# Performance work log

Measured on AMD Instinct MI355X. Metric: run time of the kernel, lower is better.

## Reference

```python
import jax, jax.numpy as jnp
import numpy as np

D = 768       # input_dim / model width
H = 3072      # expert hidden width (init arg 'output_dim')
E = 8         # num_experts
K = 2         # top_k
NOISE_STD = 0.1
B, S = 2, 1024


def setup_inputs() -> dict:
    key = jax.random.key(0)
    ks = jax.random.split(key, 16)
    sd = lambda fan_in: 1.0 / np.sqrt(fan_in)
    return {
        "x": jax.random.normal(ks[0], (B, S, D), dtype=jnp.float32),
        "noise": jax.random.normal(ks[1], (B, S, E), dtype=jnp.float32),
        # router
        "Wr": jax.random.normal(ks[2], (D, E), dtype=jnp.float32) * sd(D),
        "br": jnp.zeros((E,), dtype=jnp.float32),
        # stacked expert FFNs: d -> h -> d
        "W1": jax.random.normal(ks[3], (E, D, H), dtype=jnp.float32) * sd(D),
        "b1": jnp.zeros((E, H), dtype=jnp.float32),
        "W2": jax.random.normal(ks[4], (E, H, D), dtype=jnp.float32) * sd(H),
        "b2": jnp.zeros((E, D), dtype=jnp.float32),
        # shared expert
        "Ws1": jax.random.normal(ks[5], (D, H), dtype=jnp.float32) * sd(D),
        "bs1": jnp.zeros((H,), dtype=jnp.float32),
        "Ws2": jax.random.normal(ks[6], (H, D), dtype=jnp.float32) * sd(H),
        "bs2": jnp.zeros((D,), dtype=jnp.float32),
        # mixing scalars (alpha trainable, beta frozen in torch)
        "alpha": jnp.float32(0.3),
        "beta": jnp.float32(0.7),
    }


def reference(x, noise, Wr, br, W1, b1, W2, b2, Ws1, bs1, Ws2, bs2, alpha, beta):
    b, s, d = x.shape
    xt = x.reshape(-1, d)                       # [T, D]
    nt = noise.reshape(-1, E)                   # [T, E]
    T = xt.shape[0]

    # router: noisy logits -> top-k -> softmax over selected experts only
    logits = xt @ Wr + br + NOISE_STD * nt      # [T, E]
    top_vals, top_idx = jax.lax.top_k(logits, K)  # [T, K]
    top_w = jax.nn.softmax(top_vals, axis=-1)     # softmax over -inf-masked logits == softmax over top-k
    gates = jnp.zeros((T, E), dtype=x.dtype).at[jnp.arange(T)[:, None], top_idx].set(top_w)  # [T, E], 0 elsewhere

    # experts (dense over E; non-selected contributions are zeroed by gates)
    h = jax.nn.leaky_relu(jnp.einsum('td,edh->teh', xt, W1) + b1, negative_slope=0.01)  # [T, E, H]
    y = jnp.einsum('teh,ehd->ted', h, W2) + b2                                          # [T, E, D]
    moe_out = jnp.einsum('ted,te->td', y, gates)                                        # [T, D]

    # shared expert
    sh = jax.nn.leaky_relu(xt @ Ws1 + bs1, negative_slope=0.01)
    shared_out = sh @ Ws2 + bs2                                                         # [T, D]

    w = jax.nn.softmax(jnp.stack([alpha, beta]))
    out = shared_out * w[0] + moe_out * w[1]
    return out.reshape(b, s, d)
```

## Files before the change

kernel.cpp:

```cpp
#include <hip/hip_runtime.h>
#include <hip/hip_bf16.h>
#include <cstdio>
#include <cstdint>

#define TNUM 2048
#define DDIM 768
#define HDIM 3072
#define ENUM 8

typedef __attribute__((ext_vector_type(8))) __bf16 bf16x8;
typedef __attribute__((ext_vector_type(4))) float f32x4;
typedef __attribute__((ext_vector_type(8))) unsigned short ushort8_t;

__device__ __forceinline__ unsigned short f2bf(float f) {
    __bf16 h = (__bf16)f;
    unsigned short u;
    __builtin_memcpy(&u, &h, 2);
    return u;
}

__device__ __forceinline__ void async_cp16(const unsigned short* g, unsigned short* l) {
    __builtin_amdgcn_global_load_lds((const __attribute__((address_space(1))) void*)g,
                                     (__attribute__((address_space(3))) void*)l,
                                     16, 0, 0);
}

__global__ void cast_x_kernel(const float* __restrict__ x, unsigned short* __restrict__ xb) {
    int i = (blockIdx.x * 256 + threadIdx.x) * 8;
    float4 a = *(const float4*)(x + i);
    float4 b = *(const float4*)(x + i + 4);
    ushort4 lo = make_ushort4(f2bf(a.x), f2bf(a.y), f2bf(a.z), f2bf(a.w));
    ushort4 hi = make_ushort4(f2bf(b.x), f2bf(b.y), f2bf(b.z), f2bf(b.w));
    *(ushort4*)(xb + i) = lo;
    *(ushort4*)(xb + i + 4) = hi;
}

__global__ __launch_bounds__(256)
void transw_kernel(const float* __restrict__ W1, const float* __restrict__ W2,
                   const float* __restrict__ Ws1, const float* __restrict__ Ws2,
                   unsigned short* __restrict__ W1t, unsigned short* __restrict__ W2t,
                   unsigned short* __restrict__ Ws1t, unsigned short* __restrict__ Ws2t) {
    int z = blockIdx.z;
    const float* in; unsigned short* out; int R, C;
    if (z < 8)       { in = W1 + (size_t)z * DDIM * HDIM; out = W1t + (size_t)z * HDIM * DDIM; R = DDIM; C = HDIM; }
    else if (z < 16) { int e = z - 8; in = W2 + (size_t)e * HDIM * DDIM; out = W2t + (size_t)e * DDIM * HDIM; R = HDIM; C = DDIM; }
    else if (z == 16){ in = Ws1; out = Ws1t; R = DDIM; C = HDIM; }
    else             { in = Ws2; out = Ws2t; R = HDIM; C = DDIM; }
    int nx = C / 128;
    int c0 = (blockIdx.x % nx) * 128, r0 = (blockIdx.x / nx) * 128;
    __shared__ unsigned short tileT[128 * 136];
    int tid = threadIdx.x;
    int l15 = tid & 15;
    #pragma unroll
    for (int p = 0; p < 16; p++) {
        int unit = p * 16 + (tid >> 4);
        int r = unit >> 1, hf = unit & 1;
        int cb = hf * 64 + l15 * 4;
        float4 v = *(const float4*)(in + (size_t)(r0 + r) * C + c0 + cb);
        tileT[(cb + 0) * 136 + r] = f2bf(v.x);
        tileT[(cb + 1) * 136 + r] = f2bf(v.y);
        tileT[(cb + 2) * 136 + r] = f2bf(v.z);
        tileT[(cb + 3) * 136 + r] = f2bf(v.w);
    }
    __syncthreads();
    #pragma unroll
    for (int p = 0; p < 8; p++) {
        int cc = p * 16 + (tid >> 4);
        ushort8_t u = *(const ushort8_t*)&tileT[cc * 136 + l15 * 8];
        *(ushort8_t*)(out + (size_t)(c0 + cc) * R + r0 + l15 * 8) = u;
    }
}

__global__ void router_kernel(const float* __restrict__ x, const float* __restrict__ noise,
                              const float* __restrict__ Wr, const float* __restrict__ br,
                              int* __restrict__ counts, int* __restrict__ list,
                              int* __restrict__ inv, float* __restrict__ tokp) {
    int lane = threadIdx.x & 63;
    int t = blockIdx.x * 4 + (threadIdx.x >> 6);
    float acc[8];
    #pragma unroll
    for (int e = 0; e < 8; e++) acc[e] = 0.f;
    #pragma unroll
    for (int i = 0; i < 12; i++) {
        int d = i * 64 + lane;
        float xv = x[t * DDIM + d];
        float4 w0 = *(const float4*)(Wr + d * 8);
        float4 w1 = *(const float4*)(Wr + d * 8 + 4);
        acc[0] += xv * w0.x; acc[1] += xv * w0.y; acc[2] += xv * w0.z; acc[3] += xv * w0.w;
        acc[4] += xv * w1.x; acc[5] += xv * w1.y; acc[6] += xv * w1.z; acc[7] += xv * w1.w;
    }
    #pragma unroll
    for (int e = 0; e < 8; e++) {
        #pragma unroll
        for (int off2 = 32; off2 >= 1; off2 >>= 1)
            acc[e] += __shfl_xor(acc[e], off2, 64);
    }
    if (lane == 0) {
        float lg[8];
        #pragma unroll
        for (int e = 0; e < 8; e++) lg[e] = acc[e] + br[e] + 0.1f * noise[t * 8 + e];
        int e0 = 0;
        #pragma unroll
        for (int e = 1; e < 8; e++) if (lg[e] > lg[e0]) e0 = e;
        int e1 = -1;
        #pragma unroll
        for (int e = 0; e < 8; e++) if (e != e0 && (e1 < 0 || lg[e] > lg[e1])) e1 = e;
        float m = fmaxf(lg[e0], lg[e1]);
        float p0 = expf(lg[e0] - m), p1 = expf(lg[e1] - m);
        float inv_s = 1.f / (p0 + p1);
        int s0 = atomicAdd(&counts[e0], 1);
        list[e0 * TNUM + s0] = t;
        int s1 = atomicAdd(&counts[e1], 1);
        list[e1 * TNUM + s1] = t;
        inv[t * 2 + 0] = (e0 << 16) | s0;
        inv[t * 2 + 1] = (e1 << 16) | s1;
        tokp[t * 2 + 0] = p0 * inv_s;
        tokp[t * 2 + 1] = p1 * inv_s;
    }
}

__global__ void finalize_kernel(const int* __restrict__ counts, int* __restrict__ offs,
                                const float* __restrict__ alpha, const float* __restrict__ beta,
                                float* __restrict__ scal) {
    int s = 0;
    for (int e = 0; e < 8; e++) { offs[e] = s; s += counts[e]; }
    offs[8] = s;
    float a = alpha[0], b = beta[0];
    float m = fmaxf(a, b);
    float ea = expf(a - m), eb = expf(b - m);
    float inv = 1.f / (ea + eb);
    scal[0] = ea * inv;
    scal[1] = eb * inv;
}


__global__ __launch_bounds__(256, 4)
void ffn1_kernel(const unsigned short* __restrict__ xb,
                 const unsigned short* __restrict__ W1t,
                 const unsigned short* __restrict__ Ws1t,
                 const float* __restrict__ b1, const float* __restrict__ bs1,
                 const int* __restrict__ counts, const int* __restrict__ offs,
                 const int* __restrict__ list,
                 unsigned short* __restrict__ hbuf) {
    int j = blockIdx.z * 8 + blockIdx.x;
    if (j >= 20) return;
    int y = blockIdx.y;
    int mt = y / 12, ntl = y % 12;
    int cnt, hbase, n0, m0;
    const unsigned short* Bmat;
    const float* bias;
    const int* lst = nullptr;
    if (j < 16) {
        int e = j >> 1, nh = j & 1;
        cnt = counts[e];
        m0 = mt * 128;
        if (m0 >= cnt) return;
        hbase = offs[e];
        n0 = nh * 1536 + ntl * 128;
        Bmat = W1t + (size_t)e * HDIM * DDIM;
        bias = b1 + e * HDIM;
        lst = list + e * TNUM;
    } else {
        int q = j - 16;
        int mh = q >> 1, nh = q & 1;
        if (mt >= 8) return;
        m0 = mh * 1024 + mt * 128;
        cnt = 1 << 30;
        hbase = 2 * TNUM;
        n0 = nh * 1536 + ntl * 128;
        Bmat = Ws1t;
        bias = bs1;
    }

    __shared__ __align__(16) unsigned short As[2][512 * 8];
    __shared__ __align__(16) unsigned short Bs[2][512 * 8];

    int tid = threadIdx.x;
    int w = tid >> 6, lane = tid & 63;
    int l15 = lane & 15, quad = lane >> 4;
    int wm = (w & 1) * 64, wn = (w >> 1) * 64;

    const unsigned short* gA[2];
    const unsigned short* gB[2];
    int ldsoff[2];
    #pragma unroll
    for (int r = 0; r < 2; r++) {
        int rc = r * 4 + w;
        int rowl = rc * 16 + l15;
        int row;
        if (lst) row = lst[min(m0 + rowl, cnt - 1)];
        else     row = m0 + rowl;
        gA[r] = xb + (size_t)row * DDIM + quad * 8;
        gB[r] = Bmat + (size_t)(n0 + rowl) * DDIM + quad * 8;
        ldsoff[r] = rc * 512;
    }

    f32x4 zero = {0.f, 0.f, 0.f, 0.f};
    f32x4 acc[4][4];
    #pragma unroll
    for (int i = 0; i < 4; i++)
        #pragma unroll
        for (int jj = 0; jj < 4; jj++) acc[i][jj] = zero;

    int rcA = (w & 1) * 4;
    int rcB = (w >> 1) * 4;

    #pragma unroll
    for (int r = 0; r < 2; r++) {
        async_cp16(gA[r], &As[0][ldsoff[r]]);
        async_cp16(gB[r], &Bs[0][ldsoff[r]]);
    }

    #pragma unroll 1
    for (int kt = 0; kt < DDIM / 32; kt++) {
        __syncthreads();
        int cur = kt & 1;
        if (kt + 1 < DDIM / 32) {
            int ko = (kt + 1) * 32;
            #pragma unroll
            for (int r = 0; r < 2; r++) {
                async_cp16(gA[r] + ko, &As[cur ^ 1][ldsoff[r]]);
                async_cp16(gB[r] + ko, &Bs[cur ^ 1][ldsoff[r]]);
            }
        }
        bf16x8 af[4], bv[4];
        #pragma unroll
        for (int i = 0; i < 4; i++)
            af[i] = *(const bf16x8*)&As[cur][((rcA + i) * 64 + quad * 16 + l15) * 8];
        #pragma unroll
        for (int jj = 0; jj < 4; jj++)
            bv[jj] = *(const bf16x8*)&Bs[cur][((rcB + jj) * 64 + quad * 16 + l15) * 8];
        #pragma unroll
        for (int i = 0; i < 4; i++)
            #pragma unroll
            for (int jj = 0; jj < 4; jj++)
                acc[i][jj] = __builtin_amdgcn_mfma_f32_16x16x32_bf16(af[i], bv[jj], acc[i][jj], 0, 0, 0);
    }

    #pragma unroll
    for (int i = 0; i < 4; i++) {
        int rbase = m0 + wm + i * 16 + quad * 4;
        #pragma unroll
        for (int jj = 0; jj < 4; jj++) {
            int gc = n0 + wn + jj * 16 + l15;
            float bvl = bias[gc];
            #pragma unroll
            for (int r = 0; r < 4; r++) {
                int gr = rbase + r;
                if (gr < cnt) {
                    float v = acc[i][jj][r] + bvl;
                    v = v > 0.f ? v : 0.01f * v;
                    hbuf[(size_t)(hbase + gr) * HDIM + gc] = f2bf(v);
                }
            }
        }
    }
}

__global__ __launch_bounds__(256, 4)
void ffn2_kernel(const unsigned short* __restrict__ hbuf,
                 const unsigned short* __restrict__ W2t,
                 const unsigned short* __restrict__ Ws2t,
                 const int* __restrict__ counts, const int* __restrict__ offs,
                 float* __restrict__ ybuf) {
    int j = blockIdx.z * 8 + blockIdx.x;
    int y = blockIdx.y;
    int mt = y / 6, ntl = y % 6;
    int cnt, hbase, m0, kh;
    const unsigned short* Bmat;
    if (j < 16) {
        int e = j >> 1; kh = j & 1;
        cnt = counts[e];
        m0 = mt * 64;
        if (m0 >= cnt) return;
        hbase = offs[e];
        Bmat = W2t + (size_t)e * DDIM * HDIM;
    } else {
        int q = j - 16;
        int mh = q >> 1; kh = q & 1;
        if (mt >= 8) return;
        m0 = mh * 512 + mt * 64;
        cnt = 1 << 30;
        hbase = 2 * TNUM;
        Bmat = Ws2t;
    }
    int n0 = ntl * 128;
    int kbase = kh * (HDIM / 2);

    __shared__ __align__(16) unsigned short As[2][256 * 8];
    __shared__ __align__(16) unsigned short Bs[2][512 * 8];

    int tid = threadIdx.x;
    int w = tid >> 6, lane = tid & 63;
    int l15 = lane & 15, quad = lane >> 4;
    int wm = (w & 1) * 32, wn = (w >> 1) * 64;

    int rowl = w * 16 + l15;
    int ra = (j < 16) ? min(m0 + rowl, cnt - 1) : (m0 + rowl);
    const unsigned short* gA0 = hbuf + (size_t)(hbase + ra) * HDIM + kbase + quad * 8;
    unsigned short* lA0base0 = (unsigned short*)&As[0][w * 512];
    unsigned short* lA0base1 = (unsigned short*)&As[1][w * 512];

    const unsigned short* gB[2];
    int ldsoffB[2];
    #pragma unroll
    for (int r = 0; r < 2; r++) {
        int rc = r * 4 + w;
        gB[r] = Bmat + (size_t)(n0 + rc * 16 + l15) * HDIM + kbase + quad * 8;
        ldsoffB[r] = rc * 512;
    }

    f32x4 zero = {0.f, 0.f, 0.f, 0.f};
    f32x4 acc[2][4];
    #pragma unroll
    for (int i = 0; i < 2; i++)
        #pragma unroll
        for (int jj = 0; jj < 4; jj++) acc[i][jj] = zero;

    int rcA = (w & 1) * 2;
    int rcB = (w >> 1) * 4;

    async_cp16(gA0, lA0base0);
    #pragma unroll
    for (int r = 0; r < 2; r++) async_cp16(gB[r], &Bs[0][ldsoffB[r]]);

    const int KT = (HDIM / 2) / 32;
    #pragma unroll 1
    for (int kt = 0; kt < KT; kt++) {
        __syncthreads();
        int cur = kt & 1;
        if (kt + 1 < KT) {
            int ko = (kt + 1) * 32;
            async_cp16(gA0 + ko, cur ? lA0base0 : lA0base1);
            #pragma unroll
            for (int r = 0; r < 2; r++) async_cp16(gB[r] + ko, &Bs[cur ^ 1][ldsoffB[r]]);
        }
        bf16x8 af[2], bv[4];
        #pragma unroll
        for (int i = 0; i < 2; i++)
            af[i] = *(const bf16x8*)&As[cur][((rcA + i) * 64 + quad * 16 + l15) * 8];
        #pragma unroll
        for (int jj = 0; jj < 4; jj++)
            bv[jj] = *(const bf16x8*)&Bs[cur][((rcB + jj) * 64 + quad * 16 + l15) * 8];
        #pragma unroll
        for (int i = 0; i < 2; i++)
            #pragma unroll
            for (int jj = 0; jj < 4; jj++)
                acc[i][jj] = __builtin_amdgcn_mfma_f32_16x16x32_bf16(af[i], bv[jj], acc[i][jj], 0, 0, 0);
    }

    float* yb = ybuf + (size_t)kh * 6144 * DDIM;
    #pragma unroll
    for (int i = 0; i < 2; i++) {
        int rbase = m0 + wm + i * 16 + quad * 4;
        #pragma unroll
        for (int r = 0; r < 4; r++) {
            int gr = rbase + r;
            if (gr >= cnt) continue;
            float* orow = yb + (size_t)(hbase + gr) * DDIM + n0 + wn;
            #pragma unroll
            for (int jj = 0; jj < 4; jj++)
                orow[jj * 16 + l15] = acc[i][jj][r];
        }
    }
}

__global__ void mix_kernel(const float* __restrict__ ybuf, const int* __restrict__ inv,
                           const float* __restrict__ tokp, const int* __restrict__ offs,
                           const float* __restrict__ b2, const float* __restrict__ bs2,
                           const float* __restrict__ scal, float* __restrict__ out) {
    int t = blockIdx.x;
    int c = threadIdx.x * 4;
    int i0 = inv[t * 2 + 0], i1 = inv[t * 2 + 1];
    int e0 = i0 >> 16, sl0 = i0 & 0xFFFF;
    int e1 = i1 >> 16, sl1 = i1 & 0xFFFF;
    float p0 = tokp[t * 2 + 0], p1 = tokp[t * 2 + 1];
    float ws = scal[0], wmx = scal[1];
    size_t rA = (size_t)(offs[e0] + sl0) * DDIM + c;
    size_t rB = (size_t)(offs[e1] + sl1) * DDIM + c;
    size_t rS = (size_t)(2 * TNUM + t) * DDIM + c;
    const float* y0 = ybuf;
    const float* y1 = ybuf + (size_t)6144 * DDIM;
    float4 vA0 = *(const float4*)(y0 + rA);
    float4 vA1 = *(const float4*)(y1 + rA);
    float4 vB0 = *(const float4*)(y0 + rB);
    float4 vB1 = *(const float4*)(y1 + rB);
    float4 vS0 = *(const float4*)(y0 + rS);
    float4 vS1 = *(const float4*)(y1 + rS);
    float4 bA = *(const float4*)(b2 + e0 * DDIM + c);
    float4 bB = *(const float4*)(b2 + e1 * DDIM + c);
    float4 bS = *(const float4*)(bs2 + c);
    float4 o;
    o.x = ws * (vS0.x + vS1.x + bS.x) + wmx * (p0 * (vA0.x + vA1.x + bA.x) + p1 * (vB0.x + vB1.x + bB.x));
    o.y = ws * (vS0.y + vS1.y + bS.y) + wmx * (p0 * (vA0.y + vA1.y + bA.y) + p1 * (vB0.y + vB1.y + bB.y));
    o.z = ws * (vS0.z + vS1.z + bS.z) + wmx * (p0 * (vA0.z + vA1.z + bA.z) + p1 * (vB0.z + vB1.z + bB.z));
    o.w = ws * (vS0.w + vS1.w + bS.w) + wmx * (p0 * (vA0.w + vA1.w + bA.w) + p1 * (vB0.w + vB1.w + bB.w));
    *(float4*)(out + (size_t)t * DDIM + c) = o;
}

extern "C" void kernel_launch(void* const* d_in, const int* in_sizes, int n_in,
                              void* d_out, int out_size, void* d_ws, size_t ws_size,
                              hipStream_t stream) {
    const float* x     = (const float*)d_in[0];
    const float* noise = (const float*)d_in[1];
    const float* Wr    = (const float*)d_in[2];
    const float* br    = (const float*)d_in[3];
    const float* W1    = (const float*)d_in[4];
    const float* b1    = (const float*)d_in[5];
    const float* W2    = (const float*)d_in[6];
    const float* b2    = (const float*)d_in[7];
    const float* Ws1   = (const float*)d_in[8];
    const float* bs1   = (const float*)d_in[9];
    const float* Ws2   = (const float*)d_in[10];
    const float* bs2   = (const float*)d_in[11];
    const float* alpha = (const float*)d_in[12];
    const float* beta  = (const float*)d_in[13];

    char* ws = (char*)d_ws;
    size_t off = 0;
    auto alloc = [&](size_t bytes) -> char* {
        char* p = ws + off;
        off = (off + bytes + 255) & ~(size_t)255;
        return p;
    };
    int*   counts = (int*)  alloc(ENUM * 4);
    int*   offs   = (int*)  alloc(16 * 4);
    float* scal   = (float*)alloc(2 * 4);
    int*   list   = (int*)  alloc((size_t)ENUM * TNUM * 4);
    int*   inv    = (int*)  alloc((size_t)TNUM * 2 * 4);
    float* tokp   = (float*)alloc((size_t)TNUM * 2 * 4);
    unsigned short* xb   = (unsigned short*)alloc((size_t)TNUM * DDIM * 2);
    unsigned short* W1t  = (unsigned short*)alloc((size_t)ENUM * HDIM * DDIM * 2);
    unsigned short* Ws1t = (unsigned short*)alloc((size_t)HDIM * DDIM * 2);
    unsigned short* W2t  = (unsigned short*)alloc((size_t)ENUM * DDIM * HDIM * 2);
    unsigned short* Ws2t = (unsigned short*)alloc((size_t)DDIM * HDIM * 2);
    unsigned short* hbuf = (unsigned short*)alloc((size_t)(3 * TNUM) * HDIM * 2);
    float* ybuf = (float*)W1t;
    if (off > ws_size) {
        fprintf(stderr, "kernel_launch: workspace too small (need %zu, have %zu)\n", off, ws_size);
        return;
    }

    hipMemsetAsync(counts, 0, ENUM * 4, stream);

    cast_x_kernel<<<dim3((TNUM * DDIM / 8) / 256), dim3(256), 0, stream>>>(x, xb);
    transw_kernel<<<dim3(144, 1, 18), dim3(256), 0, stream>>>(W1, W2, Ws1, Ws2, W1t, W2t, Ws1t, Ws2t);
    router_kernel<<<dim3(TNUM / 4), dim3(256), 0, stream>>>(x, noise, Wr, br, counts, list, inv, tokp);
    finalize_kernel<<<dim3(1), dim3(1), 0, stream>>>(counts, offs, alpha, beta, scal);
    ffn1_kernel<<<dim3(8, 192, 3), dim3(256), 0, stream>>>(xb, W1t, Ws1t, b1, bs1, counts, offs, list, hbuf);
    ffn2_kernel<<<dim3(8, 192, 3), dim3(256), 0, stream>>>(hbuf, W2t, Ws2t, counts, offs, ybuf);
    mix_kernel<<<dim3(TNUM), dim3(192), 0, stream>>>(ybuf, inv, tokp, offs, b2, bs2, scal, (float*)d_out);
}
```

Before: 491.9 us.

## Triple-buffer FFN GEMM pipelines, persist M-tiles, and swizzle weight transpose LDS

Both expert GEMM kernels move from a double-buffered to a triple-buffered LDS pipeline with explicit vmcnt waits, so two K-slices are in flight at once. Grids shrink from 192 to 48 Y-blocks, and each block now loops over several M-tiles instead of launching one block per tile and exiting early on empty tiles. The weight transpose kernel packs bf16 pairs through lane shuffles and writes 32-bit words into a swizzled LDS tile to avoid bank conflicts. The costs are more LDS per block and lower occupancy (launch bounds drop from 4 to 3), plus less parallelism on experts that receive few tokens.

Result: faster. 462.3 us (-6.0%).

```diff
diff --git a/kernel.cpp b/kernel.cpp
--- a/kernel.cpp
+++ b/kernel.cpp
@@ -7,6 +7,9 @@
 #define DDIM 768
 #define HDIM 3072
 #define ENUM 8
+
+#define WAITVM(N) asm volatile("s_waitcnt vmcnt(" #N ")" ::: "memory")
+#define MEMFENCE() asm volatile("" ::: "memory")
 
 typedef __attribute__((ext_vector_type(8))) __bf16 bf16x8;
 typedef __attribute__((ext_vector_type(4))) float f32x4;
@@ -48,26 +51,45 @@
     else             { in = Ws2; out = Ws2t; R = HDIM; C = DDIM; }
     int nx = C / 128;
     int c0 = (blockIdx.x % nx) * 128, r0 = (blockIdx.x / nx) * 128;
-    __shared__ unsigned short tileT[128 * 136];
+    __shared__ __align__(16) unsigned int tileT32[128 * 68];
     int tid = threadIdx.x;
     int l15 = tid & 15;
+    int g = tid >> 4;
+    int par = (g >> 1) & 1;
+    int hf = g & 1;
+    int cb = hf * 64 + l15 * 4;
     #pragma unroll
     for (int p = 0; p < 16; p++) {
-        int unit = p * 16 + (tid >> 4);
-        int r = unit >> 1, hf = unit & 1;
-        int cb = hf * 64 + l15 * 4;
+        int unit = p * 16 + g;
+        int r = unit >> 1;
         float4 v = *(const float4*)(in + (size_t)(r0 + r) * C + c0 + cb);
-        tileT[(cb + 0) * 136 + r] = f2bf(v.x);
-        tileT[(cb + 1) * 136 + r] = f2bf(v.y);
-        tileT[(cb + 2) * 136 + r] = f2bf(v.z);
-        tileT[(cb + 3) * 136 + r] = f2bf(v.w);
+        unsigned int m01 = (unsigned int)f2bf(v.x) | ((unsigned int)f2bf(v.y) << 16);
+        unsigned int m23 = (unsigned int)f2bf(v.z) | ((unsigned int)f2bf(v.w) << 16);
+        unsigned int o01 = __shfl_xor(m01, 32);
+        unsigned int o23 = __shfl_xor(m23, 32);
+        unsigned int wA = par ? ((o23 & 0xffffu) | (m23 << 16))
+                              : ((m01 & 0xffffu) | (o01 << 16));
+        unsigned int wB = par ? ((o23 >> 16) | (m23 & 0xffff0000u))
+                              : ((m01 >> 16) | (o01 & 0xffff0000u));
+        int ca = cb + par * 2;
+        int rp = unit >> 2;
+        int cq = ca >> 2;
+        int woff = 4 * (((rp >> 2) + 3 * cq) & 15) + (((rp & 3) + cq) & 3);
+        tileT32[ca * 68 + woff] = wA;
+        tileT32[(ca + 1) * 68 + woff] = wB;
     }
     __syncthreads();
     #pragma unroll
     for (int p = 0; p < 8; p++) {
-        int cc = p * 16 + (tid >> 4);
-        ushort8_t u = *(const ushort8_t*)&tileT[cc * 136 + l15 * 8];
-        *(ushort8_t*)(out + (size_t)(c0 + cc) * R + r0 + l15 * 8) = u;
+        int cc = p * 16 + g;
+        int cqp = cc >> 2;
+        const uint4 W = *(const uint4*)&tileT32[cc * 68 + 4 * ((l15 + 3 * cqp) & 15)];
+        unsigned int a0 = W.x, a1 = W.y, a2 = W.z, a3 = W.w;
+        int rsel = cqp & 3;
+        if (rsel & 1) { unsigned int t = a0; a0 = a1; a1 = a2; a2 = a3; a3 = t; }
+        if (rsel & 2) { unsigned int t0 = a0, t1 = a1; a0 = a2; a1 = a3; a2 = t0; a3 = t1; }
+        uint4 ov; ov.x = a0; ov.y = a1; ov.z = a2; ov.w = a3;
+        *(uint4*)(out + (size_t)(c0 + cc) * R + r0 + l15 * 8) = ov;
     }
 }
 
@@ -134,7 +156,7 @@
 }
 
 
-__global__ __launch_bounds__(256, 4)
+__global__ __launch_bounds__(256, 3)
 void ffn1_kernel(const unsigned short* __restrict__ xb,
                  const unsigned short* __restrict__ W1t,
                  const unsigned short* __restrict__ Ws1t,
@@ -143,18 +165,17 @@
                  const int* __restrict__ list,
                  unsigned short* __restrict__ hbuf) {
     int j = blockIdx.z * 8 + blockIdx.x;
-    if (j >= 20) return;
     int y = blockIdx.y;
-    int mt = y / 12, ntl = y % 12;
-    int cnt, hbase, n0, m0;
+    int mt0 = y / 12, ntl = y % 12;
+    int cnt, hbase, n0, mbase, ntiles;
     const unsigned short* Bmat;
     const float* bias;
     const int* lst = nullptr;
     if (j < 16) {
         int e = j >> 1, nh = j & 1;
         cnt = counts[e];
-        m0 = mt * 128;
-        if (m0 >= cnt) return;
+        ntiles = (cnt + 127) >> 7;
+        mbase = 0;
         hbase = offs[e];
         n0 = nh * 1536 + ntl * 128;
         Bmat = W1t + (size_t)e * HDIM * DDIM;
@@ -162,95 +183,111 @@
         lst = list + e * TNUM;
     } else {
         int q = j - 16;
-        int mh = q >> 1, nh = q & 1;
-        if (mt >= 8) return;
-        m0 = mh * 1024 + mt * 128;
+        int ms = q >> 1, nh = q & 1;
+        mbase = ms * 512;
+        ntiles = 4;
         cnt = 1 << 30;
         hbase = 2 * TNUM;
         n0 = nh * 1536 + ntl * 128;
         Bmat = Ws1t;
         bias = bs1;
     }
-
-    __shared__ __align__(16) unsigned short As[2][512 * 8];
-    __shared__ __align__(16) unsigned short Bs[2][512 * 8];
+    if (mt0 >= ntiles) return;
+
+    __shared__ __align__(16) unsigned short As[3][512 * 8];
+    __shared__ __align__(16) unsigned short Bs[3][512 * 8];
 
     int tid = threadIdx.x;
     int w = tid >> 6, lane = tid & 63;
     int l15 = lane & 15, quad = lane >> 4;
     int wm = (w & 1) * 64, wn = (w >> 1) * 64;
 
-    const unsigned short* gA[2];
     const unsigned short* gB[2];
     int ldsoff[2];
+    int rowl[2];
     #pragma unroll
     for (int r = 0; r < 2; r++) {
         int rc = r * 4 + w;
-        int rowl = rc * 16 + l15;
-        int row;
-        if (lst) row = lst[min(m0 + rowl, cnt - 1)];
-        else     row = m0 + rowl;
-        gA[r] = xb + (size_t)row * DDIM + quad * 8;
-        gB[r] = Bmat + (size_t)(n0 + rowl) * DDIM + quad * 8;
+        rowl[r] = rc * 16 + l15;
+        gB[r] = Bmat + (size_t)(n0 + rowl[r]) * DDIM + quad * 8;
         ldsoff[r] = rc * 512;
     }
-
-    f32x4 zero = {0.f, 0.f, 0.f, 0.f};
-    f32x4 acc[4][4];
-    #pragma unroll
-    for (int i = 0; i < 4; i++)
-        #pragma unroll
-        for (int jj = 0; jj < 4; jj++) acc[i][jj] = zero;
-
     int rcA = (w & 1) * 4;
     int rcB = (w >> 1) * 4;
-
-    #pragma unroll
-    for (int r = 0; r < 2; r++) {
-        async_cp16(gA[r], &As[0][ldsoff[r]]);
-        async_cp16(gB[r], &Bs[0][ldsoff[r]]);
-    }
-
-    #pragma unroll 1
-    for (int kt = 0; kt < DDIM / 32; kt++) {
-        __syncthreads();
-        int cur = kt & 1;
-        if (kt + 1 < DDIM / 32) {
-            int ko = (kt + 1) * 32;
+    const int KT = DDIM / 32;
+
+    for (int mt = mt0; mt < ntiles; mt += 4) {
+        int m0 = mbase + mt * 128;
+        const unsigned short* gA[2];
+        #pragma unroll
+        for (int r = 0; r < 2; r++) {
+            int row;
+            if (lst) row = lst[min(m0 + rowl[r], cnt - 1)];
+            else     row = m0 + rowl[r];
+            gA[r] = xb + (size_t)row * DDIM + quad * 8;
+        }
+
+        f32x4 zero = {0.f, 0.f, 0.f, 0.f};
+        f32x4 acc[4][4];
+        #pragma unroll
+        for (int i = 0; i < 4; i++)
+            #pragma unroll
+            for (int jj = 0; jj < 4; jj++) acc[i][jj] = zero;
+
+        __builtin_amdgcn_s_barrier();
+        MEMFENCE();
+        #pragma unroll
+        for (int t = 0; t < 2; t++)
             #pragma unroll
             for (int r = 0; r < 2; r++) {
-                async_cp16(gA[r] + ko, &As[cur ^ 1][ldsoff[r]]);
-                async_cp16(gB[r] + ko, &Bs[cur ^ 1][ldsoff[r]]);
+                async_cp16(gA[r] + t * 32, &As[t][ldsoff[r]]);
+                async_cp16(gB[r] + t * 32, &Bs[t][ldsoff[r]]);
             }
-        }
-        bf16x8 af[4], bv[4];
-        #pragma unroll
-        for (int i = 0; i < 4; i++)
-            af[i] = *(const bf16x8*)&As[cur][((rcA + i) * 64 + quad * 16 + l15) * 8];
-        #pragma unroll
-        for (int jj = 0; jj < 4; jj++)
-            bv[jj] = *(const bf16x8*)&Bs[cur][((rcB + jj) * 64 + quad * 16 + l15) * 8];
-        #pragma unroll
-        for (int i = 0; i < 4; i++)
+
+        #pragma unroll 1
+        for (int kt = 0; kt < KT; kt++) {
+            if (kt == KT - 1) { WAITVM(0); } else { WAITVM(4); }
+            __builtin_amdgcn_s_barrier();
+            MEMFENCE();
+            int cur = kt % 3;
+            if (kt + 2 < KT) {
+                int nb = (kt + 2) % 3;
+                int ko = (kt + 2) * 32;
+                #pragma unroll
+                for (int r = 0; r < 2; r++) {
+                    async_cp16(gA[r] + ko, &As[nb][ldsoff[r]]);
+                    async_cp16(gB[r] + ko, &Bs[nb][ldsoff[r]]);
+                }
+            }
+            bf16x8 af[4], bv[4];
+            #pragma unroll
+            for (int i = 0; i < 4; i++)
+                af[i] = *(const bf16x8*)&As[cur][((rcA + i) * 64 + quad * 16 + l15) * 8];
             #pragma unroll
             for (int jj = 0; jj < 4; jj++)
-                acc[i][jj] = __builtin_amdgcn_mfma_f32_16x16x32_bf16(af[i], bv[jj], acc[i][jj], 0, 0, 0);
-    }
-
-    #pragma unroll
-    for (int i = 0; i < 4; i++) {
-        int rbase = m0 + wm + i * 16 + quad * 4;
-        #pragma unroll
-        for (int jj = 0; jj < 4; jj++) {
-            int gc = n0 + wn + jj * 16 + l15;
-            float bvl = bias[gc];
-            #pragma unroll
-            for (int r = 0; r < 4; r++) {
-                int gr = rbase + r;
-                if (gr < cnt) {
-                    float v = acc[i][jj][r] + bvl;
-                    v = v > 0.f ? v : 0.01f * v;
-                    hbuf[(size_t)(hbase + gr) * HDIM + gc] = f2bf(v);
+                bv[jj] = *(const bf16x8*)&Bs[cur][((rcB + jj) * 64 + quad * 16 + l15) * 8];
+            #pragma unroll
+            for (int i = 0; i < 4; i++)
+                #pragma unroll
+                for (int jj = 0; jj < 4; jj++)
+                    acc[i][jj] = __builtin_amdgcn_mfma_f32_16x16x32_bf16(af[i], bv[jj], acc[i][jj], 0, 0, 0);
+        }
+
+        #pragma unroll
+        for (int i = 0; i < 4; i++) {
+            int rbase = m0 + wm + i * 16 + quad * 4;
+            #pragma unroll
+            for (int jj = 0; jj < 4; jj++) {
+                int gc = n0 + wn + jj * 16 + l15;
+                float bvl = bias[gc];
+                #pragma unroll
+                for (int r = 0; r < 4; r++) {
+                    int gr = rbase + r;
+                    if (gr < cnt) {
+                        float v = acc[i][jj][r] + bvl;
+                        v = v > 0.f ? v : 0.01f * v;
+                        hbuf[(size_t)(hbase + gr) * HDIM + gc] = f2bf(v);
+                    }
                 }
             }
         }
@@ -265,42 +302,37 @@
                  float* __restrict__ ybuf) {
     int j = blockIdx.z * 8 + blockIdx.x;
     int y = blockIdx.y;
-    int mt = y / 6, ntl = y % 6;
-    int cnt, hbase, m0, kh;
+    int mt0 = y / 6, ntl = y % 6;
+    int cnt, hbase, mbase, kh, ntiles;
     const unsigned short* Bmat;
     if (j < 16) {
         int e = j >> 1; kh = j & 1;
         cnt = counts[e];
-        m0 = mt * 64;
-        if (m0 >= cnt) return;
+        ntiles = (cnt + 63) >> 6;
+        mbase = 0;
         hbase = offs[e];
         Bmat = W2t + (size_t)e * DDIM * HDIM;
     } else {
         int q = j - 16;
         int mh = q >> 1; kh = q & 1;
-        if (mt >= 8) return;
-        m0 = mh * 512 + mt * 64;
+        mbase = mh * 512;
+        ntiles = 8;
         cnt = 1 << 30;
         hbase = 2 * TNUM;
         Bmat = Ws2t;
     }
+    if (mt0 >= ntiles) return;
     int n0 = ntl * 128;
     int kbase = kh * (HDIM / 2);
 
-    __shared__ __align__(16) unsigned short As[2][256 * 8];
-    __shared__ __align__(16) unsigned short Bs[2][512 * 8];
+    __shared__ __align__(16) unsigned short As[3][256 * 8];
+    __shared__ __align__(16) unsigned short Bs[3][512 * 8];
 
     int tid = threadIdx.x;
     int w = tid >> 6, lane = tid & 63;
     int l15 = lane & 15, quad = lane >> 4;
     int wm = (w & 1) * 32, wn = (w >> 1) * 64;
 
-    int rowl = w * 16 + l15;
-    int ra = (j < 16) ? min(m0 + rowl, cnt - 1) : (m0 + rowl);
-    const unsigned short* gA0 = hbuf + (size_t)(hbase + ra) * HDIM + kbase + quad * 8;
-    unsigned short* lA0base0 = (unsigned short*)&As[0][w * 512];
-    unsigned short* lA0base1 = (unsigned short*)&As[1][w * 512];
-
     const unsigned short* gB[2];
     int ldsoffB[2];
     #pragma unroll
@@ -309,58 +341,72 @@
         gB[r] = Bmat + (size_t)(n0 + rc * 16 + l15) * HDIM + kbase + quad * 8;
         ldsoffB[r] = rc * 512;
     }
-
-    f32x4 zero = {0.f, 0.f, 0.f, 0.f};
-    f32x4 acc[2][4];
-    #pragma unroll
-    for (int i = 0; i < 2; i++)
-        #pragma unroll
-        for (int jj = 0; jj < 4; jj++) acc[i][jj] = zero;
-
     int rcA = (w & 1) * 2;
     int rcB = (w >> 1) * 4;
-
-    async_cp16(gA0, lA0base0);
-    #pragma unroll
-    for (int r = 0; r < 2; r++) async_cp16(gB[r], &Bs[0][ldsoffB[r]]);
-
     const int KT = (HDIM / 2) / 32;
-    #pragma unroll 1
-    for (int kt = 0; kt < KT; kt++) {
-        __syncthreads();
-        int cur = kt & 1;
-        if (kt + 1 < KT) {
-            int ko = (kt + 1) * 32;
-            async_cp16(gA0 + ko, cur ? lA0base0 : lA0base1);
-            #pragma unroll
-            for (int r = 0; r < 2; r++) async_cp16(gB[r] + ko, &Bs[cur ^ 1][ldsoffB[r]]);
-        }
-        bf16x8 af[2], bv[4];
+    int rowl = w * 16 + l15;
+    float* yb = ybuf + (size_t)kh * 6144 * DDIM;
+
+    for (int mt = mt0; mt < ntiles; mt += 8) {
+        int m0 = mbase + mt * 64;
+        int ra = (j < 16) ? min(m0 + rowl, cnt - 1) : (m0 + rowl);
+        const unsigned short* gA0 = hbuf + (size_t)(hbase + ra) * HDIM + kbase + quad * 8;
+
+        f32x4 zero = {0.f, 0.f, 0.f, 0.f};
+        f32x4 acc[2][4];
         #pragma unroll
         for (int i = 0; i < 2; i++)
-            af[i] = *(const bf16x8*)&As[cur][((rcA + i) * 64 + quad * 16 + l15) * 8];
-        #pragma unroll
-        for (int jj = 0; jj < 4; jj++)
-            bv[jj] = *(const bf16x8*)&Bs[cur][((rcB + jj) * 64 + quad * 16 + l15) * 8];
-        #pragma unroll
-        for (int i = 0; i < 2; i++)
+            #pragma unroll
+            for (int jj = 0; jj < 4; jj++) acc[i][jj] = zero;
+
+        __builtin_amdgcn_s_barrier();
+        MEMFENCE();
+        #pragma unroll
+        for (int t = 0; t < 2; t++) {
+            async_cp16(gA0 + t * 32, &As[t][w * 512]);
+            #pragma unroll
+            for (int r = 0; r < 2; r++) async_cp16(gB[r] + t * 32, &Bs[t][ldsoffB[r]]);
+        }
+
+        #pragma unroll 1
+        for (int kt = 0; kt < KT; kt++) {
+            if (kt == KT - 1) { WAITVM(0); } else { WAITVM(3); }
+            __builtin_amdgcn_s_barrier();
+            MEMFENCE();
+            int cur = kt % 3;
+            if (kt + 2 < KT) {
+                int nb = (kt + 2) % 3;
+                int ko = (kt + 2) * 32;
+                async_cp16(gA0 + ko, &As[nb][w * 512]);
+                #pragma unroll
+                for (int r = 0; r < 2; r++) async_cp16(gB[r] + ko, &Bs[nb][ldsoffB[r]]);
+            }
+            bf16x8 af[2], bv[4];
+            #pragma unroll
+            for (int i = 0; i < 2; i++)
+                af[i] = *(const bf16x8*)&As[cur][((rcA + i) * 64 + quad * 16 + l15) * 8];
             #pragma unroll
             for (int jj = 0; jj < 4; jj++)
-                acc[i][jj] = __builtin_amdgcn_mfma_f32_16x16x32_bf16(af[i], bv[jj], acc[i][jj], 0, 0, 0);
-    }
-
-    float* yb = ybuf + (size_t)kh * 6144 * DDIM;
-    #pragma unroll
-    for (int i = 0; i < 2; i++) {
-        int rbase = m0 + wm + i * 16 + quad * 4;
-        #pragma unroll
-        for (int r = 0; r < 4; r++) {
-            int gr = rbase + r;
-            if (gr >= cnt) continue;
-            float* orow = yb + (size_t)(hbase + gr) * DDIM + n0 + wn;
-            #pragma unroll
-            for (int jj = 0; jj < 4; jj++)
-                orow[jj * 16 + l15] = acc[i][jj][r];
+                bv[jj] = *(const bf16x8*)&Bs[cur][((rcB + jj) * 64 + quad * 16 + l15) * 8];
+            #pragma unroll
+            for (int i = 0; i < 2; i++)
+                #pragma unroll
+                for (int jj = 0; jj < 4; jj++)
+                    acc[i][jj] = __builtin_amdgcn_mfma_f32_16x16x32_bf16(af[i], bv[jj], acc[i][jj], 0, 0, 0);
+        }
+
+        #pragma unroll
+        for (int i = 0; i < 2; i++) {
+            int rbase = m0 + wm + i * 16 + quad * 4;
+            #pragma unroll
+            for (int r = 0; r < 4; r++) {
+                int gr = rbase + r;
+                if (gr >= cnt) continue;
+                float* orow = yb + (size_t)(hbase + gr) * DDIM + n0 + wn;
+                #pragma unroll
+                for (int jj = 0; jj < 4; jj++)
+                    orow[jj * 16 + l15] = acc[i][jj][r];
+            }
         }
     }
 }
@@ -447,7 +493,7 @@
     transw_kernel<<<dim3(144, 1, 18), dim3(256), 0, stream>>>(W1, W2, Ws1, Ws2, W1t, W2t, Ws1t, Ws2t);
     router_kernel<<<dim3(TNUM / 4), dim3(256), 0, stream>>>(x, noise, Wr, br, counts, list, inv, tokp);
     finalize_kernel<<<dim3(1), dim3(1), 0, stream>>>(counts, offs, alpha, beta, scal);
-    ffn1_kernel<<<dim3(8, 192, 3), dim3(256), 0, stream>>>(xb, W1t, Ws1t, b1, bs1, counts, offs, list, hbuf);
-    ffn2_kernel<<<dim3(8, 192, 3), dim3(256), 0, stream>>>(hbuf, W2t, Ws2t, counts, offs, ybuf);
+    ffn1_kernel<<<dim3(8, 48, 3), dim3(256), 0, stream>>>(xb, W1t, Ws1t, b1, bs1, counts, offs, list, hbuf);
+    ffn2_kernel<<<dim3(8, 48, 3), dim3(256), 0, stream>>>(hbuf, W2t, Ws2t, counts, offs, ybuf);
     mix_kernel<<<dim3(TNUM), dim3(192), 0, stream>>>(ybuf, inv, tokp, offs, b2, bs2, scal, (float*)d_out);
 }
```
